# Kernel optimization log

Measured on AMD Instinct MI355X. Metric: run time of the kernel, lower is better.

Reference implementation:

```python
import jax, jax.numpy as jnp
import numpy as np
import math

DEFAULT_MASK_VALUE = -0.7 * float(np.finfo(np.float32).max)
WINDOW_SIZE = 256


def _slide_attn_mask(length, window_size, dtype):
    # _compute_slide_attn_mask with w == length (no query chunking):
    # offset = min(window_size, 0) = 0 -> m1 = triu(k=1) (causal part),
    # window_size >= length - w = 0 -> m2 = tril(k=-window_size) (window part)
    x = jnp.ones((length, length), dtype=jnp.float32)
    m = jnp.triu(x, k=1) + jnp.tril(x, k=-window_size)
    m = jnp.where(m > 0.5, DEFAULT_MASK_VALUE, 0.0).astype(dtype)
    return m[None, None]  # [1, 1, T, S]


def _cross_head_proj(x, w, qw1, qw2, kw1, kw2, qdd, kdd):
    # x: [B, H, T, S] attention logits/probs; w: [G, M, M] static mixing
    # qw1/qw2: [B, T, G, M, I], kw1/kw2: [B, S, G, M, I], qdd/kdd: [B, T(S), G, M]
    B, H, T, S = x.shape
    G = w.shape[0]
    M = H // G
    inp = x.reshape(B, G, M, T, S)
    ret = inp + jnp.einsum('BGMTS,GMN->BGNTS', inp, w)  # residual + static proj
    I = qw1.shape[-1]  # dynamic hidden dim (<= 2, loop_over_dynamic_hd path)
    for i in range(I):
        h = jnp.einsum('BGMTS,BTGM->BGTS', inp, qw1[..., i])  # query-wise squeeze
        ret = ret + jnp.einsum('BGTS,BTGM->BGMTS', h, qw2[..., i])
        h = jnp.einsum('BGMTS,BSGM->BGTS', inp, kw1[..., i])  # key-wise squeeze
        ret = ret + jnp.einsum('BGTS,BSGM->BGMTS', h, kw2[..., i])
    # dynamic diagonal (per-head gating) terms
    ret = ret + jnp.einsum('BGMTS,BTGM->BGMTS', inp, qdd)
    ret = ret + jnp.einsum('BGMTS,BSGM->BGMTS', inp, kdd)
    return ret.reshape(B, H, T, S)


def setup_inputs() -> dict:
    key = jax.random.key(0)
    ks = jax.random.split(key, 20)
    B, T, N, D = 2, 1024, 16, 128
    G, M, I = 1, 16, 2
    w_scale = math.sqrt(2.0 / (M + M)) * 0.1  # init_fn relative_scale=0.1 path
    dyn_scale = 0.05
    inp = {
        'q': jax.random.normal(ks[0], (B, T, N, D), jnp.float32),
        'k': jax.random.normal(ks[1], (B, T, N, D), jnp.float32),
        'v': jax.random.normal(ks[2], (B, T, N, D), jnp.float32),
        'w_pre': jax.random.normal(ks[3], (G, M, M), jnp.float32) * w_scale,
        'w_post': jax.random.normal(ks[4], (G, M, M), jnp.float32) * w_scale,
    }
    names = ['qw1_pre', 'qw2_pre', 'kw1_pre', 'kw2_pre',
             'qw1_post', 'qw2_post', 'kw1_post', 'kw2_post']
    for j, name in enumerate(names):
        inp[name] = jax.random.normal(ks[5 + j], (B, T, G, M, I), jnp.float32) * dyn_scale
    for j, name in enumerate(['qdd_pre', 'kdd_pre', 'qdd_post', 'kdd_post']):
        inp[name] = jax.random.normal(ks[13 + j], (B, T, G, M), jnp.float32) * dyn_scale
    return inp


def reference(q, k, v, w_pre, w_post,
              qw1_pre, qw2_pre, kw1_pre, kw2_pre,
              qw1_post, qw2_post, kw1_post, kw2_post,
              qdd_pre, kdd_pre, qdd_post, kdd_post):
    B, T, N, D = q.shape
    logits = jnp.einsum('btnh,bsnh->bnts', q, k) / jnp.sqrt(jnp.asarray(D, q.dtype))
    # pre-softmax cross-head projection
    logits = _cross_head_proj(logits, w_pre, qw1_pre, qw2_pre, kw1_pre, kw2_pre,
                              qdd_pre, kdd_pre)
    mask = _slide_attn_mask(T, WINDOW_SIZE, logits.dtype)
    # apply_mask_to_logits: predicate-based masking (avoids bad add-fusion)
    logits = jnp.where(mask >= DEFAULT_MASK_VALUE * 0.5, logits, DEFAULT_MASK_VALUE)
    probs = jax.nn.softmax(logits, axis=-1)
    # post-softmax cross-head projection
    probs = _cross_head_proj(probs, w_post, qw1_post, qw2_post, kw1_post, kw2_post,
                             qdd_post, kdd_post)
    return jnp.einsum('bnts,bsnh->btnh', probs, v)
```

## Files before the change

kernel.cpp:

```cpp
#include <hip/hip_runtime.h>

#define TT 1024
#define NH 16
#define DD 128
#define WIN 256
#define SW 288
#define SCALE 0.08838834764831845f

typedef float f32x4 __attribute__((ext_vector_type(4)));
typedef short s16x8 __attribute__((ext_vector_type(8)));

__device__ __forceinline__ ushort f2bf(float x) {
  union { float f; unsigned u; } v; v.f = x;
  unsigned r = v.u + 0x7FFFu + ((v.u >> 16) & 1u);
  return (ushort)(r >> 16);
}
__device__ __forceinline__ float bf2f(ushort u) {
  union { unsigned u; float f; } v; v.u = ((unsigned)u) << 16; return v.f;
}
__device__ __forceinline__ float bflo(uint p) {
  union { unsigned u; float f; } v; v.u = p << 16; return v.f;
}
__device__ __forceinline__ float bfhi(uint p) {
  union { unsigned u; float f; } v; v.u = p & 0xFFFF0000u; return v.f;
}

__global__ __launch_bounds__(256)
void prep_big(const float* __restrict__ q, const float* __restrict__ k,
              const float* __restrict__ v,
              ushort* __restrict__ qb8, ushort* __restrict__ kb8, ushort* __restrict__ v8)
{
  const int g = blockIdx.x;
  const int tid = threadIdx.x;
  __shared__ float sB[64 * 132];
  if (g < 1024) {
    const float* src = (g < 512) ? q : k;
    ushort* dst = (g < 512) ? qb8 : kb8;
    const float scale = (g < 512) ? SCALE : 1.0f;
    const int bidx = g & 511;
    const int tt = bidx & 15, h = (bidx >> 4) & 15, b = bidx >> 8;
    const int t0 = tt * 64;
#pragma unroll
    for (int it = 0; it < 8; ++it) {
      int idx = tid + it * 256;
      int r = idx >> 5, cg = idx & 31;
      float4 x = *(const float4*)(src + (((long long)(b * TT + t0 + r)) * NH + h) * DD + cg * 4);
      *(float4*)(&sB[r * 132 + cg * 4]) = x;
    }
    __syncthreads();
#pragma unroll
    for (int it = 0; it < 4; ++it) {
      int idx = tid + it * 256;
      int t = idx & 63, doct = idx >> 6;
      union { ushort u[8]; uint4 v; } pk;
#pragma unroll
      for (int e = 0; e < 8; ++e)
        pk.u[e] = f2bf(sB[t * 132 + doct * 8 + e] * scale);
      *(uint4*)(dst + ((((long long)(b * NH + h)) * 16 + doct) * TT + t0 + t) * 8) = pk.v;
    }
  } else {
    const int bidx = g - 1024;
    const int st = bidx & 15, h = (bidx >> 4) & 15, b = bidx >> 8;
    const int s0 = st * 64;
#pragma unroll
    for (int it = 0; it < 8; ++it) {
      int idx = tid + it * 256;
      int r = idx >> 5, cg = idx & 31;
      float4 x = *(const float4*)(v + (((long long)(b * TT + s0 + r)) * NH + h) * DD + cg * 4);
      *(float4*)(&sB[r * 132 + cg * 4]) = x;
    }
    __syncthreads();
#pragma unroll
    for (int it = 0; it < 4; ++it) {
      int idx = tid + it * 256;
      int d = idx & 127, so = idx >> 7;
      union { ushort u[8]; uint4 v; } pk;
#pragma unroll
      for (int e = 0; e < 8; ++e)
        pk.u[e] = f2bf(sB[(so * 8 + e) * 132 + d]);
      *(uint4*)(v8 + ((((long long)(b * NH + h)) * 128 + st * 8 + so) * DD + d) * 8) = pk.v;
    }
  }
}

__global__ __launch_bounds__(256)
void prep_small(const float* __restrict__ w_pre, const float* __restrict__ w_post,
                const float* __restrict__ qw1_pre, const float* __restrict__ qw2_pre,
                const float* __restrict__ qdd_pre,
                const float* __restrict__ kw1_pre, const float* __restrict__ kw2_pre,
                const float* __restrict__ kdd_pre,
                const float* __restrict__ qw1_post, const float* __restrict__ qw2_post,
                const float* __restrict__ qdd_post,
                const float* __restrict__ kw1_post, const float* __restrict__ kw2_post,
                const float* __restrict__ kdd_post,
                uint* __restrict__ mqA, uint* __restrict__ kwsT2)
{
  const int g = blockIdx.x;
  const int tid = threadIdx.x;
  if (g < 4096) {
    __shared__ ushort sH[256];
    const int t = g & 1023, b = (g >> 10) & 1, pass = g >> 11;
    const float* W   = pass ? w_post   : w_pre;
    const float* QW1 = pass ? qw1_post : qw1_pre;
    const float* QW2 = pass ? qw2_post : qw2_pre;
    const float* QDD = pass ? qdd_post : qdd_pre;
    const int m = tid >> 4, n = tid & 15;
    const long long bt = (long long)b * TT + t;
    float val = W[tid]
              + QW1[bt * 32 + 2 * m] * QW2[bt * 32 + 2 * n]
              + QW1[bt * 32 + 2 * m + 1] * QW2[bt * 32 + 2 * n + 1];
    if (m == n) val += QDD[bt * 16 + n];
    sH[((m >> 2) * 16 + n) * 4 + (m & 3)] = f2bf(val);
    __syncthreads();
    if (tid < 128)
      mqA[(((long long)(pass * 2 + b) * TT + t)) * 128 + tid] =
          (uint)sH[2 * tid] | ((uint)sH[2 * tid + 1] << 16);
  } else {
    __shared__ float sKW[64][84];
    const int bidx = g - 4096;
    const int sch = bidx & 15, b = (bidx >> 4) & 1, pass = bidx >> 5;
    const int s0b = sch * 64;
    const float* KW1 = pass ? kw1_post : kw1_pre;
    const float* KW2 = pass ? kw2_post : kw2_pre;
    const float* KDD = pass ? kdd_post : kdd_pre;
#pragma unroll
    for (int k2 = 0; k2 < 5; ++k2) {
      int idx = tid + k2 * 256;
      int s = idx / 20, q4 = idx % 20;
      long long bs = (long long)b * TT + s0b + s;
      float4 vv; int dst;
      if (q4 < 8)       { vv = ((const float4*)(KW1 + bs * 32))[q4];      dst = q4 * 4; }
      else if (q4 < 16) { vv = ((const float4*)(KW2 + bs * 32))[q4 - 8];  dst = 32 + (q4 - 8) * 4; }
      else              { vv = ((const float4*)(KDD + bs * 16))[q4 - 16]; dst = 64 + (q4 - 16) * 4; }
      *(float4*)(&sKW[s][dst]) = vv;
    }
    __syncthreads();
#pragma unroll
    for (int k2 = 0; k2 < 10; ++k2) {
      int idx = tid + k2 * 256;
      int j2 = idx >> 6, s = idx & 63;
      uint pr = (uint)f2bf(sKW[s][2 * j2]) | ((uint)f2bf(sKW[s][2 * j2 + 1]) << 16);
      kwsT2[((long long)(pass * 2 + b) * 40 + j2) * 1024 + s0b + s] = pr;
    }
  }
}

__global__ __launch_bounds__(256, 4)
void ka_qk(const ushort* __restrict__ qb8, const ushort* __restrict__ kb8,
           ushort* __restrict__ S)
{
  const int tid = threadIdx.x;
  const int raw = blockIdx.x;
  const int job = (raw & 7) * 128 + (raw >> 3);
  const int b = job >> 9, h = (job >> 5) & 15, tt = job & 31;
  const int t0 = tt * 32;
  const int s0 = (t0 >= WIN) ? t0 - WIN : 0;
  const int lane = tid & 63, wv = tid >> 6;

  __shared__ float strip[16 * 300];

  const ushort* qbase = qb8 + ((long long)(b * NH + h)) * 16 * (TT * 8);
  const ushort* kbase = kb8 + ((long long)(b * NH + h)) * 16 * (TT * 8);

  for (int rt = 0; rt < 2; ++rt) {
    const int tlo = t0 + rt * 16;
    s16x8 qa[4];
    {
      const int trow = tlo + (lane & 15);
      const int ko = lane >> 4;
#pragma unroll
      for (int kk = 0; kk < 4; ++kk)
        qa[kk] = *(const s16x8*)(qbase + ((long long)(kk * 4 + ko)) * (TT * 8) + trow * 8);
    }
    int cl0 = tlo - (WIN - 1) - s0; if (cl0 < 0) cl0 = 0;
    const int chi = tlo + 15 - s0;
    const int stb = cl0 >> 4;
    const int nst = (chi >> 4) - stb + 1;
    for (int sti = wv; sti < nst; sti += 4) {
      const int cst = (stb + sti) * 16;
      const int scol = s0 + cst + (lane & 15);
      const int ko = lane >> 4;
      f32x4 acc = {0.f, 0.f, 0.f, 0.f};
#pragma unroll
      for (int kk = 0; kk < 4; ++kk) {
        s16x8 kb = *(const s16x8*)(kbase + ((long long)(kk * 4 + ko)) * (TT * 8) + scol * 8);
        acc = __builtin_amdgcn_mfma_f32_16x16x32_bf16(qa[kk], kb, acc, 0, 0, 0);
      }
      const int r0 = (lane >> 4) * 4;
#pragma unroll
      for (int j = 0; j < 4; ++j)
        strip[(r0 + j) * 300 + cst + (lane & 15)] = acc[j];
    }
    __syncthreads();
    const long long srow0 = (((long long)(b * NH + h)) * TT + tlo) * SW;
#pragma unroll
    for (int it = 0; it < 3; ++it) {
      int idx = tid + it * 256;
      if (idx < 16 * 36) {
        int r = idx / 36, sg = idx % 36;
        union { ushort u[8]; uint4 v; } pk;
#pragma unroll
        for (int e = 0; e < 8; ++e)
          pk.u[e] = f2bf(strip[r * 300 + sg * 8 + e]);
        *(uint4*)(S + srow0 + (long long)r * SW + sg * 8) = pk.v;
      }
    }
    __syncthreads();
  }
}

__global__ __launch_bounds__(256, 2)
void kb_proj(const uint* __restrict__ mqA, const uint* __restrict__ kwsT2,
             ushort* __restrict__ S)
{
  const int tid = threadIdx.x;
  const int raw = blockIdx.x;
  const int job = (raw & 7) * 64 + (raw >> 3);
  const int b = job >> 8, tq = job & 255;
  const int t0 = tq * 4;
  const int t32 = t0 & ~31;
  const int s0 = (t32 >= WIN) ? t32 - WIN : 0;
  const int lane = tid & 63, wv = tid >> 6;
  const int t = t0 + wv;
  const int q = lane >> 4, cl = lane & 15;
  const int n0 = 4 * q;

  __shared__ uint skw[40][292];

  s16x8 aPre, aPost;
  {
    uint2 a1 = *(const uint2*)(mqA + (((long long)b * TT + t) * 128) + lane * 2);
    uint2 a2 = *(const uint2*)(mqA + (((long long)(2 + b) * TT + t) * 128) + lane * 2);
    union { uint u[4]; s16x8 v; } pk;
    pk.u[0] = a1.x; pk.u[1] = a1.y; pk.u[2] = 0; pk.u[3] = 0; aPre = pk.v;
    pk.u[0] = a2.x; pk.u[1] = a2.y; aPost = pk.v;
  }

  const uint* kwb1 = kwsT2 + (long long)b * (40 * 1024);
  const uint* kwb2 = kwsT2 + (long long)(2 + b) * (40 * 1024);
#define STAGE(BASE)                                                          \
  { _Pragma("unroll") for (int i = 0; i < 12; ++i) {                         \
      int idx = tid + i * 256;                                               \
      if (idx < 2880) {                                                      \
        int j2 = idx / 72, s4 = idx % 72;                                    \
        uint4 vv = *(const uint4*)((BASE) + (long long)j2 * 1024 + s0 + s4 * 4); \
        *(uint4*)(&skw[j2][s4 * 4]) = vv; } } }

  STAGE(kwb1);
  __syncthreads();

  const ushort* Sbt = S + ((long long)b * NH) * (TT * SW) + (long long)t * SW;
  uint usv[18][2];
  float zp[4] = {0.f, 0.f, 0.f, 0.f};

#pragma unroll
  for (int g = 0; g < 18; ++g) {
    const int c = g * 16 + cl;
    const int sg = s0 + c;
    ushort u0 = Sbt[(long long)(n0 + 0) * (TT * SW) + c];
    ushort u1 = Sbt[(long long)(n0 + 1) * (TT * SW) + c];
    ushort u2 = Sbt[(long long)(n0 + 2) * (TT * SW) + c];
    ushort u3 = Sbt[(long long)(n0 + 3) * (TT * SW) + c];
    union { uint u[4]; s16x8 v; } bf;
    bf.u[0] = (uint)u0 | ((uint)u1 << 16);
    bf.u[1] = (uint)u2 | ((uint)u3 << 16);
    bf.u[2] = 0; bf.u[3] = 0;
    f32x4 acc = {0.f, 0.f, 0.f, 0.f};
    acc = __builtin_amdgcn_mfma_f32_16x16x32_bf16(aPre, bf.v, acc, 0, 0, 0);
    float f0 = bf2f(u0), f1 = bf2f(u1), f2 = bf2f(u2), f3 = bf2f(u3);
    uint w0 = skw[n0 + 0][c], w1 = skw[n0 + 1][c], w2 = skw[n0 + 2][c], w3 = skw[n0 + 3][c];
    float hk0 = f0 * bflo(w0) + f1 * bflo(w1) + f2 * bflo(w2) + f3 * bflo(w3);
    float hk1 = f0 * bfhi(w0) + f1 * bfhi(w1) + f2 * bfhi(w2) + f3 * bfhi(w3);
    hk0 += __shfl_xor(hk0, 16); hk0 += __shfl_xor(hk0, 32);
    hk1 += __shfl_xor(hk1, 16); hk1 += __shfl_xor(hk1, 32);
    const bool valid = (sg <= t) && (sg + WIN > t);
    uint k20 = skw[16 + n0 + 0][c], k21 = skw[16 + n0 + 1][c];
    uint k22 = skw[16 + n0 + 2][c], k23 = skw[16 + n0 + 3][c];
    uint kd0 = skw[32 + 2 * q][c], kd1 = skw[32 + 2 * q + 1][c];
    float x0 = acc[0] + f0 + hk0 * bflo(k20) + hk1 * bfhi(k20) + f0 * bflo(kd0);
    float x1 = acc[1] + f1 + hk0 * bflo(k21) + hk1 * bfhi(k21) + f1 * bfhi(kd0);
    float x2 = acc[2] + f2 + hk0 * bflo(k22) + hk1 * bfhi(k22) + f2 * bflo(kd1);
    float x3 = acc[3] + f3 + hk0 * bflo(k23) + hk1 * bfhi(k23) + f3 * bfhi(kd1);
    float e0 = valid ? __expf(x0) : 0.f;
    float e1 = valid ? __expf(x1) : 0.f;
    float e2 = valid ? __expf(x2) : 0.f;
    float e3 = valid ? __expf(x3) : 0.f;
    zp[0] += e0; zp[1] += e1; zp[2] += e2; zp[3] += e3;
    usv[g][0] = (uint)f2bf(e0) | ((uint)f2bf(e1) << 16);
    usv[g][1] = (uint)f2bf(e2) | ((uint)f2bf(e3) << 16);
  }

  float rz[4];
#pragma unroll
  for (int j = 0; j < 4; ++j) {
    float z = zp[j];
    z += __shfl_xor(z, 1); z += __shfl_xor(z, 2);
    z += __shfl_xor(z, 4); z += __shfl_xor(z, 8);
    rz[j] = 1.0f / z;
  }

  __syncthreads();
  STAGE(kwb2);
  __syncthreads();

#pragma unroll
  for (int g = 0; g < 18; ++g) {
    const int c = g * 16 + cl;
    float p0 = bflo(usv[g][0]) * rz[0];
    float p1 = bfhi(usv[g][0]) * rz[1];
    float p2 = bflo(usv[g][1]) * rz[2];
    float p3 = bfhi(usv[g][1]) * rz[3];
    union { uint u[4]; s16x8 v; } bf;
    bf.u[0] = (uint)f2bf(p0) | ((uint)f2bf(p1) << 16);
    bf.u[1] = (uint)f2bf(p2) | ((uint)f2bf(p3) << 16);
    bf.u[2] = 0; bf.u[3] = 0;
    f32x4 acc = {0.f, 0.f, 0.f, 0.f};
    acc = __builtin_amdgcn_mfma_f32_16x16x32_bf16(aPost, bf.v, acc, 0, 0, 0);
    uint w0 = skw[n0 + 0][c], w1 = skw[n0 + 1][c], w2 = skw[n0 + 2][c], w3 = skw[n0 + 3][c];
    float hk0 = p0 * bflo(w0) + p1 * bflo(w1) + p2 * bflo(w2) + p3 * bflo(w3);
    float hk1 = p0 * bfhi(w0) + p1 * bfhi(w1) + p2 * bfhi(w2) + p3 * bfhi(w3);
    hk0 += __shfl_xor(hk0, 16); hk0 += __shfl_xor(hk0, 32);
    hk1 += __shfl_xor(hk1, 16); hk1 += __shfl_xor(hk1, 32);
    uint k20 = skw[16 + n0 + 0][c], k21 = skw[16 + n0 + 1][c];
    uint k22 = skw[16 + n0 + 2][c], k23 = skw[16 + n0 + 3][c];
    uint kd0 = skw[32 + 2 * q][c], kd1 = skw[32 + 2 * q + 1][c];
    float x0 = acc[0] + p0 + hk0 * bflo(k20) + hk1 * bfhi(k20) + p0 * bflo(kd0);
    float x1 = acc[1] + p1 + hk0 * bflo(k21) + hk1 * bfhi(k21) + p1 * bfhi(kd0);
    float x2 = acc[2] + p2 + hk0 * bflo(k22) + hk1 * bfhi(k22) + p2 * bflo(kd1);
    float x3 = acc[3] + p3 + hk0 * bflo(k23) + hk1 * bfhi(k23) + p3 * bfhi(kd1);
    ushort* So = (ushort*)Sbt;
    So[(long long)(n0 + 0) * (TT * SW) + c] = f2bf(x0);
    So[(long long)(n0 + 1) * (TT * SW) + c] = f2bf(x1);
    So[(long long)(n0 + 2) * (TT * SW) + c] = f2bf(x2);
    So[(long long)(n0 + 3) * (TT * SW) + c] = f2bf(x3);
  }
}

__global__ __launch_bounds__(256, 4)
void kc_pv(const ushort* __restrict__ S, const ushort* __restrict__ v8,
           float* __restrict__ out)
{
  const int tid = threadIdx.x;
  const int raw = blockIdx.x;
  const int job = (raw & 7) * 128 + (raw >> 3);
  const int b = job >> 9, h = (job >> 5) & 15, tt = job & 31;
  const int t0 = tt * 32;
  const int s0 = (t0 >= WIN) ? t0 - WIN : 0;
  const int lane = tid & 63, wv = tid >> 6;

  __shared__ ushort sPt[32 * 296];

  const long long prow0 = (((long long)(b * NH + h)) * TT + t0) * SW;
#pragma unroll
  for (int it = 0; it < 5; ++it) {
    int idx = tid + it * 256;
    if (idx < 32 * 36) {
      int r = idx / 36, sg = idx % 36;
      uint4 v = *(const uint4*)(S + prow0 + (long long)r * SW + sg * 8);
      *(uint4*)(&sPt[r * 296 + sg * 8]) = v;
    }
  }
  __syncthreads();

  const ushort* vbase = v8 + ((long long)(b * NH + h)) * (128 * DD * 8)
                           + ((long long)(s0 >> 3)) * (DD * 8);
  const int dcol = lane & 15, soct = lane >> 4;
  const int dt0 = wv * 2;
  f32x4 acc[2][2];
#pragma unroll
  for (int rt = 0; rt < 2; ++rt)
#pragma unroll
    for (int dd = 0; dd < 2; ++dd) acc[rt][dd] = (f32x4){0.f, 0.f, 0.f, 0.f};

#pragma unroll
  for (int ks = 0; ks < 9; ++ks) {
    s16x8 a0 = *(const s16x8*)(&sPt[(dcol) * 296 + ks * 32 + soct * 8]);
    s16x8 a1 = *(const s16x8*)(&sPt[(16 + dcol) * 296 + ks * 32 + soct * 8]);
#pragma unroll
    for (int dd = 0; dd < 2; ++dd) {
      s16x8 vb = *(const s16x8*)(vbase + (((long long)(ks * 4 + soct)) * DD + (dt0 + dd) * 16 + dcol) * 8);
      acc[0][dd] = __builtin_amdgcn_mfma_f32_16x16x32_bf16(a0, vb, acc[0][dd], 0, 0, 0);
      acc[1][dd] = __builtin_amdgcn_mfma_f32_16x16x32_bf16(a1, vb, acc[1][dd], 0, 0, 0);
    }
  }
  const int r0 = (lane >> 4) * 4;
#pragma unroll
  for (int rt = 0; rt < 2; ++rt)
#pragma unroll
    for (int dd = 0; dd < 2; ++dd)
#pragma unroll
      for (int j = 0; j < 4; ++j) {
        int trow = t0 + rt * 16 + r0 + j;
        out[(((long long)(b * TT + trow)) * NH + h) * DD + (dt0 + dd) * 16 + dcol] = acc[rt][dd][j];
      }
}

extern "C" void kernel_launch(void* const* d_in, const int* in_sizes, int n_in,
                              void* d_out, int out_size, void* d_ws, size_t ws_size,
                              hipStream_t stream) {
  const float* q        = (const float*)d_in[0];
  const float* k        = (const float*)d_in[1];
  const float* v        = (const float*)d_in[2];
  const float* w_pre    = (const float*)d_in[3];
  const float* w_post   = (const float*)d_in[4];
  const float* qw1_pre  = (const float*)d_in[5];
  const float* qw2_pre  = (const float*)d_in[6];
  const float* kw1_pre  = (const float*)d_in[7];
  const float* kw2_pre  = (const float*)d_in[8];
  const float* qw1_post = (const float*)d_in[9];
  const float* qw2_post = (const float*)d_in[10];
  const float* kw1_post = (const float*)d_in[11];
  const float* kw2_post = (const float*)d_in[12];
  const float* qdd_pre  = (const float*)d_in[13];
  const float* kdd_pre  = (const float*)d_in[14];
  const float* qdd_post = (const float*)d_in[15];
  const float* kdd_post = (const float*)d_in[16];
  float* out = (float*)d_out;

  ushort* qb8   = (ushort*)d_ws;
  ushort* kb8   = (ushort*)((char*)d_ws + 8388608ll);
  ushort* v8    = (ushort*)((char*)d_ws + 16777216ll);
  ushort* S     = (ushort*)((char*)d_ws + 25165824ll);
  uint*   mqA   = (uint*)  ((char*)d_ws + 44040192ll);
  uint*   kwsT2 = (uint*)  ((char*)d_ws + 46137344ll);

  prep_big  <<<1536, 256, 0, stream>>>(q, k, v, qb8, kb8, v8);
  prep_small<<<4160, 256, 0, stream>>>(w_pre, w_post,
                                       qw1_pre, qw2_pre, qdd_pre, kw1_pre, kw2_pre, kdd_pre,
                                       qw1_post, qw2_post, qdd_post, kw1_post, kw2_post, kdd_post,
                                       mqA, kwsT2);
  ka_qk     <<<1024, 256, 0, stream>>>(qb8, kb8, S);
  kb_proj   <<<512, 256, 0, stream>>>(mqA, kwsT2, S);
  kc_pv     <<<1024, 256, 0, stream>>>(S, v8, out);
}
```

Measured before the change: 64.18 us.

## Merge prep kernels into one launch and split kb_proj columns across two half-blocks

Folds prep_big and prep_small into a single prep_all launch, which removes one kernel launch and its tail. The mqA branch now handles 8 timesteps per block instead of 1, so far fewer tiny blocks are launched. kb_proj goes to 512 threads, and two waves share each query row, each covering half of the 18 column groups. Their softmax partial sums are combined through shared memory. The aim is to cut per-thread register and serial work and raise parallelism, at the cost of an extra shared-memory reduction.

```diff
diff --git a/kernel.cpp b/kernel.cpp
--- a/kernel.cpp
+++ b/kernel.cpp
@@ -26,13 +26,23 @@
 }
 
 __global__ __launch_bounds__(256)
-void prep_big(const float* __restrict__ q, const float* __restrict__ k,
+void prep_all(const float* __restrict__ q, const float* __restrict__ k,
               const float* __restrict__ v,
-              ushort* __restrict__ qb8, ushort* __restrict__ kb8, ushort* __restrict__ v8)
+              const float* __restrict__ w_pre, const float* __restrict__ w_post,
+              const float* __restrict__ qw1_pre, const float* __restrict__ qw2_pre,
+              const float* __restrict__ qdd_pre,
+              const float* __restrict__ kw1_pre, const float* __restrict__ kw2_pre,
+              const float* __restrict__ kdd_pre,
+              const float* __restrict__ qw1_post, const float* __restrict__ qw2_post,
+              const float* __restrict__ qdd_post,
+              const float* __restrict__ kw1_post, const float* __restrict__ kw2_post,
+              const float* __restrict__ kdd_post,
+              ushort* __restrict__ qb8, ushort* __restrict__ kb8, ushort* __restrict__ v8,
+              uint* __restrict__ mqA, uint* __restrict__ kwsT2)
 {
   const int g = blockIdx.x;
   const int tid = threadIdx.x;
-  __shared__ float sB[64 * 132];
+  __shared__ float sPool[64 * 132];
   if (g < 1024) {
     const float* src = (g < 512) ? q : k;
     ushort* dst = (g < 512) ? qb8 : kb8;
@@ -45,7 +55,7 @@
       int idx = tid + it * 256;
       int r = idx >> 5, cg = idx & 31;
       float4 x = *(const float4*)(src + (((long long)(b * TT + t0 + r)) * NH + h) * DD + cg * 4);
-      *(float4*)(&sB[r * 132 + cg * 4]) = x;
+      *(float4*)(&sPool[r * 132 + cg * 4]) = x;
     }
     __syncthreads();
 #pragma unroll
@@ -55,10 +65,10 @@
       union { ushort u[8]; uint4 v; } pk;
 #pragma unroll
       for (int e = 0; e < 8; ++e)
-        pk.u[e] = f2bf(sB[t * 132 + doct * 8 + e] * scale);
+        pk.u[e] = f2bf(sPool[t * 132 + doct * 8 + e] * scale);
       *(uint4*)(dst + ((((long long)(b * NH + h)) * 16 + doct) * TT + t0 + t) * 8) = pk.v;
     }
-  } else {
+  } else if (g < 1536) {
     const int bidx = g - 1024;
     const int st = bidx & 15, h = (bidx >> 4) & 15, b = bidx >> 8;
     const int s0 = st * 64;
@@ -67,7 +77,7 @@
       int idx = tid + it * 256;
       int r = idx >> 5, cg = idx & 31;
       float4 x = *(const float4*)(v + (((long long)(b * TT + s0 + r)) * NH + h) * DD + cg * 4);
-      *(float4*)(&sB[r * 132 + cg * 4]) = x;
+      *(float4*)(&sPool[r * 132 + cg * 4]) = x;
     }
     __syncthreads();
 #pragma unroll
@@ -77,47 +87,41 @@
       union { ushort u[8]; uint4 v; } pk;
 #pragma unroll
       for (int e = 0; e < 8; ++e)
-        pk.u[e] = f2bf(sB[(so * 8 + e) * 132 + d]);
+        pk.u[e] = f2bf(sPool[(so * 8 + e) * 132 + d]);
       *(uint4*)(v8 + ((((long long)(b * NH + h)) * 128 + st * 8 + so) * DD + d) * 8) = pk.v;
     }
-  }
-}
-
-__global__ __launch_bounds__(256)
-void prep_small(const float* __restrict__ w_pre, const float* __restrict__ w_post,
-                const float* __restrict__ qw1_pre, const float* __restrict__ qw2_pre,
-                const float* __restrict__ qdd_pre,
-                const float* __restrict__ kw1_pre, const float* __restrict__ kw2_pre,
-                const float* __restrict__ kdd_pre,
-                const float* __restrict__ qw1_post, const float* __restrict__ qw2_post,
-                const float* __restrict__ qdd_post,
-                const float* __restrict__ kw1_post, const float* __restrict__ kw2_post,
-                const float* __restrict__ kdd_post,
-                uint* __restrict__ mqA, uint* __restrict__ kwsT2)
-{
-  const int g = blockIdx.x;
-  const int tid = threadIdx.x;
-  if (g < 4096) {
-    __shared__ ushort sH[256];
-    const int t = g & 1023, b = (g >> 10) & 1, pass = g >> 11;
+  } else if (g < 2048) {
+    ushort* sH = (ushort*)sPool;
+    const int gg = g - 1536;
+    const int tgrp = gg & 127, b = (gg >> 7) & 1, pass = gg >> 8;
+    const int t0 = tgrp * 8;
     const float* W   = pass ? w_post   : w_pre;
     const float* QW1 = pass ? qw1_post : qw1_pre;
     const float* QW2 = pass ? qw2_post : qw2_pre;
     const float* QDD = pass ? qdd_post : qdd_pre;
-    const int m = tid >> 4, n = tid & 15;
-    const long long bt = (long long)b * TT + t;
-    float val = W[tid]
-              + QW1[bt * 32 + 2 * m] * QW2[bt * 32 + 2 * n]
-              + QW1[bt * 32 + 2 * m + 1] * QW2[bt * 32 + 2 * n + 1];
-    if (m == n) val += QDD[bt * 16 + n];
-    sH[((m >> 2) * 16 + n) * 4 + (m & 3)] = f2bf(val);
-    __syncthreads();
-    if (tid < 128)
-      mqA[(((long long)(pass * 2 + b) * TT + t)) * 128 + tid] =
-          (uint)sH[2 * tid] | ((uint)sH[2 * tid + 1] << 16);
+    const int tl = tid >> 5, j = tid & 31;
+    const long long bt = (long long)b * TT + t0 + tl;
+#pragma unroll
+    for (int ee = 0; ee < 8; ++ee) {
+      int e = ee * 32 + j;
+      int n = e & 15, m = e >> 4;
+      float val = W[e]
+                + QW1[bt * 32 + 2 * m] * QW2[bt * 32 + 2 * n]
+                + QW1[bt * 32 + 2 * m + 1] * QW2[bt * 32 + 2 * n + 1];
+      if (m == n) val += QDD[bt * 16 + n];
+      sH[tl * 256 + ((m >> 2) * 16 + n) * 4 + (m & 3)] = f2bf(val);
+    }
+    __syncthreads();
+#pragma unroll
+    for (int kk = 0; kk < 4; ++kk) {
+      int idx = tid + kk * 256;
+      int tl2 = idx >> 7, off = idx & 127;
+      mqA[(((long long)(pass * 2 + b) * TT + t0 + tl2)) * 128 + off] =
+          (uint)sH[tl2 * 256 + 2 * off] | ((uint)sH[tl2 * 256 + 2 * off + 1] << 16);
+    }
   } else {
-    __shared__ float sKW[64][84];
-    const int bidx = g - 4096;
+    float (*sKW)[84] = (float (*)[84])sPool;
+    const int bidx = g - 2048;
     const int sch = bidx & 15, b = (bidx >> 4) & 1, pass = bidx >> 5;
     const int s0b = sch * 64;
     const float* KW1 = pass ? kw1_post : kw1_pre;
@@ -209,7 +213,7 @@
   }
 }
 
-__global__ __launch_bounds__(256, 2)
+__global__ __launch_bounds__(512, 2)
 void kb_proj(const uint* __restrict__ mqA, const uint* __restrict__ kwsT2,
              ushort* __restrict__ S)
 {
@@ -221,11 +225,13 @@
   const int t32 = t0 & ~31;
   const int s0 = (t32 >= WIN) ? t32 - WIN : 0;
   const int lane = tid & 63, wv = tid >> 6;
-  const int t = t0 + wv;
+  const int t = t0 + (wv & 3);
+  const int half = wv >> 2;
   const int q = lane >> 4, cl = lane & 15;
   const int n0 = 4 * q;
 
   __shared__ uint skw[40][292];
+  __shared__ float sZp[8][4][4];
 
   s16x8 aPre, aPost;
   {
@@ -239,8 +245,8 @@
   const uint* kwb1 = kwsT2 + (long long)b * (40 * 1024);
   const uint* kwb2 = kwsT2 + (long long)(2 + b) * (40 * 1024);
 #define STAGE(BASE)                                                          \
-  { _Pragma("unroll") for (int i = 0; i < 12; ++i) {                         \
-      int idx = tid + i * 256;                                               \
+  { _Pragma("unroll") for (int i = 0; i < 6; ++i) {                          \
+      int idx = tid + i * 512;                                               \
       if (idx < 2880) {                                                      \
         int j2 = idx / 72, s4 = idx % 72;                                    \
         uint4 vv = *(const uint4*)((BASE) + (long long)j2 * 1024 + s0 + s4 * 4); \
@@ -250,12 +256,13 @@
   __syncthreads();
 
   const ushort* Sbt = S + ((long long)b * NH) * (TT * SW) + (long long)t * SW;
-  uint usv[18][2];
+  uint usv[9][2];
   float zp[4] = {0.f, 0.f, 0.f, 0.f};
 
 #pragma unroll
-  for (int g = 0; g < 18; ++g) {
-    const int c = g * 16 + cl;
+  for (int i = 0; i < 9; ++i) {
+    const int gg = half * 9 + i;
+    const int c = gg * 16 + cl;
     const int sg = s0 + c;
     ushort u0 = Sbt[(long long)(n0 + 0) * (TT * SW) + c];
     ushort u1 = Sbt[(long long)(n0 + 1) * (TT * SW) + c];
@@ -286,30 +293,37 @@
     float e2 = valid ? __expf(x2) : 0.f;
     float e3 = valid ? __expf(x3) : 0.f;
     zp[0] += e0; zp[1] += e1; zp[2] += e2; zp[3] += e3;
-    usv[g][0] = (uint)f2bf(e0) | ((uint)f2bf(e1) << 16);
-    usv[g][1] = (uint)f2bf(e2) | ((uint)f2bf(e3) << 16);
-  }
-
-  float rz[4];
+    usv[i][0] = (uint)f2bf(e0) | ((uint)f2bf(e1) << 16);
+    usv[i][1] = (uint)f2bf(e2) | ((uint)f2bf(e3) << 16);
+  }
+
 #pragma unroll
   for (int j = 0; j < 4; ++j) {
     float z = zp[j];
     z += __shfl_xor(z, 1); z += __shfl_xor(z, 2);
     z += __shfl_xor(z, 4); z += __shfl_xor(z, 8);
-    rz[j] = 1.0f / z;
-  }
-
+    zp[j] = z;
+  }
+  if (cl == 0) {
+#pragma unroll
+    for (int j = 0; j < 4; ++j) sZp[wv][q][j] = zp[j];
+  }
   __syncthreads();
+  float rz[4];
+#pragma unroll
+  for (int j = 0; j < 4; ++j)
+    rz[j] = 1.0f / (sZp[wv][q][j] + sZp[wv ^ 4][q][j]);
   STAGE(kwb2);
   __syncthreads();
 
 #pragma unroll
-  for (int g = 0; g < 18; ++g) {
-    const int c = g * 16 + cl;
-    float p0 = bflo(usv[g][0]) * rz[0];
-    float p1 = bfhi(usv[g][0]) * rz[1];
-    float p2 = bflo(usv[g][1]) * rz[2];
-    float p3 = bfhi(usv[g][1]) * rz[3];
+  for (int i = 0; i < 9; ++i) {
+    const int gg = half * 9 + i;
+    const int c = gg * 16 + cl;
+    float p0 = bflo(usv[i][0]) * rz[0];
+    float p1 = bfhi(usv[i][0]) * rz[1];
+    float p2 = bflo(usv[i][1]) * rz[2];
+    float p3 = bfhi(usv[i][1]) * rz[3];
     union { uint u[4]; s16x8 v; } bf;
     bf.u[0] = (uint)f2bf(p0) | ((uint)f2bf(p1) << 16);
     bf.u[1] = (uint)f2bf(p2) | ((uint)f2bf(p3) << 16);
@@ -424,12 +438,12 @@
   uint*   mqA   = (uint*)  ((char*)d_ws + 44040192ll);
   uint*   kwsT2 = (uint*)  ((char*)d_ws + 46137344ll);
 
-  prep_big  <<<1536, 256, 0, stream>>>(q, k, v, qb8, kb8, v8);
-  prep_small<<<4160, 256, 0, stream>>>(w_pre, w_post,
-                                       qw1_pre, qw2_pre, qdd_pre, kw1_pre, kw2_pre, kdd_pre,
-                                       qw1_post, qw2_post, qdd_post, kw1_post, kw2_post, kdd_post,
-                                       mqA, kwsT2);
-  ka_qk     <<<1024, 256, 0, stream>>>(qb8, kb8, S);
-  kb_proj   <<<512, 256, 0, stream>>>(mqA, kwsT2, S);
-  kc_pv     <<<1024, 256, 0, stream>>>(S, v8, out);
-}
+  prep_all<<<2112, 256, 0, stream>>>(q, k, v,
+                                     w_pre, w_post,
+                                     qw1_pre, qw2_pre, qdd_pre, kw1_pre, kw2_pre, kdd_pre,
+                                     qw1_post, qw2_post, qdd_post, kw1_post, kw2_post, kdd_post,
+                                     qb8, kb8, v8, mqA, kwsT2);
+  ka_qk  <<<1024, 256, 0, stream>>>(qb8, kb8, S);
+  kb_proj<<<512, 512, 0, stream>>>(mqA, kwsT2, S);
+  kc_pv  <<<1024, 256, 0, stream>>>(S, v8, out);
+}
```

Result: faster. 58.39 us (-9.0%).
